# Optimization experiments

Hardware: AMD Instinct MI355X
Metric: run time of the kernel (lower is better)

The kernel has to match this reference:

```python
import jax, jax.numpy as jnp
import numpy as np


def log_g(x):
    # log of g(x) where g(x) = x + 0.5 for x >= 0 else sigmoid(x)
    return jnp.where(x >= 0, jnp.log(jnp.where(x >= 0, x, 0.0) + 0.5), -jax.nn.softplus(-x))


def mingru_layer(x, h0, W, b):
    # x: (B,S,Din), h0: (B,1,H) positive, W: (2H,Din), b: (2H,)
    gh = jnp.einsum('bsd,ed->bse', x, W) + b
    gate, hidden = jnp.split(gh, 2, axis=-1)
    log_z = -jax.nn.softplus(-gate)        # log sigmoid(gate)
    log_coeffs = -jax.nn.softplus(gate)    # log (1 - sigmoid(gate))
    log_values = jnp.concatenate([jnp.log(h0), log_z + log_g(hidden)], axis=1)  # (B,S+1,H)
    a_star = jnp.pad(jnp.cumsum(log_coeffs, axis=1), ((0, 0), (1, 0), (0, 0)))  # (B,S+1,H)
    log_h = a_star + jax.lax.cumlogsumexp(log_values - a_star, axis=1)
    return jnp.exp(log_h)[:, 1:]  # (B,S,H)


def setup_inputs() -> dict:
    key = jax.random.key(0)
    ks = jax.random.split(key, 6)
    B, S, D, H = 8, 2048, 1024, 1024
    L = 2
    s = 0.02
    return {
        'x': jax.random.normal(ks[0], (B, S, D), jnp.float32),
        'h': jax.random.uniform(ks[1], (L, B, 1, H), jnp.float32, 0.05, 1.0),
        'w0': jax.random.normal(ks[2], (2 * H, D), jnp.float32) * s,
        'b0': jax.random.normal(ks[3], (2 * H,), jnp.float32) * s,
        'w1': jax.random.normal(ks[4], (2 * H, H), jnp.float32) * s,
        'b1': jax.random.normal(ks[5], (2 * H,), jnp.float32) * s,
    }


def reference(x, h, w0, b0, w1, b1):
    # layer 0 (residual, align = Identity since input_dims == hidden_dims)
    out0 = mingru_layer(x, h[0], w0, b0)
    h0_final = out0[:, -1:]
    inp = out0 + x
    # layer 1 (last layer: residual, no dropout after)
    out1 = mingru_layer(inp, h[1], w1, b1)
    h1_final = out1[:, -1:]
    out = out1 + inp
    h_final = jnp.stack([h0_final, h1_final])  # (L,B,1,H)
    return out, h_final
```

## Files before the change

kernel.cpp:

```cpp
#include <hip/hip_runtime.h>
#include <hip/hip_bf16.h>
#include <cstdint>
#include <cstddef>

#define GAS __attribute__((address_space(1)))
#define LAS __attribute__((address_space(3)))

typedef __attribute__((ext_vector_type(8))) __bf16 bf16x8;
typedef __attribute__((ext_vector_type(4))) float f32x4;

constexpr int kB = 8, kS = 2048, kK = 1024, kH = 1024;
constexpr int kM = kB * kS;
constexpr int kN2 = 2 * kH;
constexpr int kChunks = 64;
constexpr int kSc = kS / kChunks;

constexpr size_t kOffXb   = 0;
constexpr size_t kOffW0   = 33554432;
constexpr size_t kOffW1   = 37748736;
constexpr size_t kOffA    = 41943040;
constexpr size_t kOffG    = 75497472;
constexpr size_t kOffCA   = 109051904;
constexpr size_t kOffCV   = 111149056;
constexpr size_t kOffHst  = 113246208;
constexpr size_t kWsNeed  = 115343360;

__device__ __forceinline__ ushort f2bf(float f) {
    union { float f; uint32_t u; } v; v.f = f;
    uint32_t r = v.u + 0x7FFFu + ((v.u >> 16) & 1u);
    return (ushort)(r >> 16);
}
__device__ __forceinline__ float bf2f(ushort u) {
    union { uint32_t u; float f; } v; v.u = (uint32_t)u << 16;
    return v.f;
}

__global__ void cvt_bf16_kernel(const float* __restrict__ src, ushort* __restrict__ dst, int n4) {
    int i = blockIdx.x * blockDim.x + threadIdx.x;
    if (i >= n4) return;
    f32x4 v = *reinterpret_cast<const f32x4*>(src + (size_t)i * 4);
    ushort4 o;
    o.x = f2bf(v.x); o.y = f2bf(v.y); o.z = f2bf(v.z); o.w = f2bf(v.w);
    *reinterpret_cast<ushort4*>(dst + (size_t)i * 4) = o;
}

__global__ __launch_bounds__(256, 2)
void gemm_epi_kernel(const ushort* __restrict__ A, const ushort* __restrict__ W,
                     const float* __restrict__ bias,
                     ushort* __restrict__ abuf, ushort* __restrict__ gbuf)
{
    __shared__ ushort As[128 * 64];
    __shared__ ushort Bs[128 * 64];

    const int tid  = threadIdx.x;
    const int lane = tid & 63;
    const int wv   = tid >> 6;
    const int bid  = blockIdx.x;
    const int tn   = bid & 15;
    const int tm   = bid >> 4;
    const int m0   = tm * 128;
    const int n0   = tn * 128;
    const int wm   = wv & 1, wn = wv >> 1;

    f32x4 acc[4][4];
#pragma unroll
    for (int i = 0; i < 4; ++i)
#pragma unroll
        for (int j = 0; j < 4; ++j) acc[i][j] = (f32x4){0.f, 0.f, 0.f, 0.f};

    const int srow = tid >> 3;
    const int scol = (tid & 7) * 8;
    const size_t a_base = (size_t)(m0 + srow) * kK + scol;
    const size_t b_base = (size_t)(n0 + srow) * kK + scol;

    for (int kt = 0; kt < kK / 64; ++kt) {
        const int k0 = kt * 64;
#pragma unroll
        for (int i = 0; i < 4; ++i) {
            const ushort* gp = A + a_base + (size_t)i * 32 * kK + k0;
            __builtin_amdgcn_global_load_lds((const GAS void*)gp,
                (LAS void*)((char*)As + i * 4096 + wv * 1024), 16, 0, 0);
        }
#pragma unroll
        for (int i = 0; i < 4; ++i) {
            const ushort* gp = W + b_base + (size_t)i * 32 * kK + k0;
            __builtin_amdgcn_global_load_lds((const GAS void*)gp,
                (LAS void*)((char*)Bs + i * 4096 + wv * 1024), 16, 0, 0);
        }
        __syncthreads();
#pragma unroll
        for (int ks = 0; ks < 2; ++ks) {
            bf16x8 af[4], bfr[4];
#pragma unroll
            for (int mr = 0; mr < 4; ++mr) {
                int off = (wm * 64 + mr * 16 + (lane & 15)) * 64 + ks * 32 + (lane >> 4) * 8;
                af[mr] = *reinterpret_cast<const bf16x8*>(&As[off]);
            }
#pragma unroll
            for (int nr = 0; nr < 4; ++nr) {
                int off = (wn * 64 + nr * 16 + (lane & 15)) * 64 + ks * 32 + (lane >> 4) * 8;
                bfr[nr] = *reinterpret_cast<const bf16x8*>(&Bs[off]);
            }
#pragma unroll
            for (int mr = 0; mr < 4; ++mr)
#pragma unroll
                for (int nr = 0; nr < 4; ++nr)
                    acc[mr][nr] = __builtin_amdgcn_mfma_f32_16x16x32_bf16(af[mr], bfr[nr], acc[mr][nr], 0, 0, 0);
        }
        __syncthreads();
    }

    const bool isGate = (tn < 8);
    ushort* outp = isGate ? abuf : gbuf;
    const int nb_local = (isGate ? tn : tn - 8) * 128 + wn * 64;
    float bn[4];
#pragma unroll
    for (int nr = 0; nr < 4; ++nr) bn[nr] = bias[n0 + wn * 64 + nr * 16 + (lane & 15)];
#pragma unroll
    for (int mr = 0; mr < 4; ++mr) {
#pragma unroll
        for (int i = 0; i < 4; ++i) {
            const int m = m0 + wm * 64 + mr * 16 + (lane >> 4) * 4 + i;
            ushort* rowp = outp + (size_t)m * kH + nb_local;
#pragma unroll
            for (int nr = 0; nr < 4; ++nr) {
                float val = acc[mr][nr][i] + bn[nr];
                float r;
                if (isGate) r = 1.f / (1.f + __expf(val));
                else        r = (val >= 0.f) ? val + 0.5f : 1.f / (1.f + __expf(-val));
                rowp[nr * 16 + (lane & 15)] = f2bf(r);
            }
        }
    }
}

__global__ void scan_reduce_kernel(const ushort* __restrict__ abuf, const ushort* __restrict__ gbuf,
                                   float* __restrict__ cA, float* __restrict__ cV)
{
    int idx = blockIdx.x * 256 + threadIdx.x;
    int chg = idx & 255;
    int c   = (idx >> 8) & (kChunks - 1);
    int b   = idx >> 14;
    size_t ch = (size_t)chg * 4;
    size_t row = (size_t)b * kS + (size_t)c * kSc;
    const ushort* ap = abuf + row * kH + ch;
    const ushort* gp = gbuf + row * kH + ch;
    f32x4 A = (f32x4){1.f, 1.f, 1.f, 1.f};
    f32x4 V = (f32x4){0.f, 0.f, 0.f, 0.f};
    for (int t = 0; t < kSc; ++t) {
        ushort4 au = *reinterpret_cast<const ushort4*>(ap);
        ushort4 gu = *reinterpret_cast<const ushort4*>(gp);
        f32x4 a = (f32x4){bf2f(au.x), bf2f(au.y), bf2f(au.z), bf2f(au.w)};
        f32x4 g = (f32x4){bf2f(gu.x), bf2f(gu.y), bf2f(gu.z), bf2f(gu.w)};
        V = a * V + (1.f - a) * g;
        A = A * a;
        ap += kH; gp += kH;
    }
    size_t o = ((size_t)(b * kChunks + c) * kH) + ch;
    *reinterpret_cast<f32x4*>(cA + o) = A;
    *reinterpret_cast<f32x4*>(cV + o) = V;
}

__global__ void scan_chunks_kernel(const float* __restrict__ cA, const float* __restrict__ cV,
                                   const float* __restrict__ h0, float* __restrict__ hstart,
                                   float* __restrict__ hfin)
{
    int idx = blockIdx.x * 256 + threadIdx.x;
    int chg = idx & 255;
    int b   = idx >> 8;
    size_t ch = (size_t)chg * 4;
    f32x4 h = *reinterpret_cast<const f32x4*>(h0 + (size_t)b * kH + ch);
    for (int c = 0; c < kChunks; ++c) {
        size_t o = ((size_t)(b * kChunks + c) * kH) + ch;
        *reinterpret_cast<f32x4*>(hstart + o) = h;
        f32x4 A = *reinterpret_cast<const f32x4*>(cA + o);
        f32x4 V = *reinterpret_cast<const f32x4*>(cV + o);
        h = A * h + V;
    }
    *reinterpret_cast<f32x4*>(hfin + (size_t)b * kH + ch) = h;
}

template<bool L1>
__global__ void scan_apply_kernel(const ushort* __restrict__ abuf, const ushort* __restrict__ gbuf,
                                  const float* __restrict__ hstart, const void* __restrict__ addin,
                                  void* __restrict__ outp)
{
    int idx = blockIdx.x * 256 + threadIdx.x;
    int chg = idx & 255;
    int c   = (idx >> 8) & (kChunks - 1);
    int b   = idx >> 14;
    size_t ch = (size_t)chg * 4;
    size_t row = (size_t)b * kS + (size_t)c * kSc;
    size_t base = row * kH + ch;
    f32x4 h = *reinterpret_cast<const f32x4*>(hstart + ((size_t)(b * kChunks + c) * kH) + ch);
    const ushort* ap = abuf + base;
    const ushort* gp = gbuf + base;
    for (int t = 0; t < kSc; ++t) {
        ushort4 au = *reinterpret_cast<const ushort4*>(ap);
        ushort4 gu = *reinterpret_cast<const ushort4*>(gp);
        f32x4 a = (f32x4){bf2f(au.x), bf2f(au.y), bf2f(au.z), bf2f(au.w)};
        f32x4 g = (f32x4){bf2f(gu.x), bf2f(gu.y), bf2f(gu.z), bf2f(gu.w)};
        h = a * h + (1.f - a) * g;
        f32x4 r;
        if (L1) {
            ushort4 xu = *reinterpret_cast<const ushort4*>((const ushort*)addin + base + (size_t)t * kH);
            r = (f32x4){bf2f(xu.x), bf2f(xu.y), bf2f(xu.z), bf2f(xu.w)};
        } else {
            r = *reinterpret_cast<const f32x4*>((const float*)addin + base + (size_t)t * kH);
        }
        f32x4 o = h + r;
        if (L1) {
            *reinterpret_cast<f32x4*>((float*)outp + base + (size_t)t * kH) = o;
        } else {
            ushort4 ob;
            ob.x = f2bf(o.x); ob.y = f2bf(o.y); ob.z = f2bf(o.z); ob.w = f2bf(o.w);
            *reinterpret_cast<ushort4*>((ushort*)outp + base + (size_t)t * kH) = ob;
        }
        ap += kH; gp += kH;
    }
}

extern "C" void kernel_launch(void* const* d_in, const int* in_sizes, int n_in,
                              void* d_out, int out_size, void* d_ws, size_t ws_size,
                              hipStream_t stream)
{
    const float* x  = (const float*)d_in[0];
    const float* h  = (const float*)d_in[1];
    const float* w0 = (const float*)d_in[2];
    const float* b0 = (const float*)d_in[3];
    const float* w1 = (const float*)d_in[4];
    const float* b1 = (const float*)d_in[5];
    float* out = (float*)d_out;
    char* ws = (char*)d_ws;

    if (ws_size < kWsNeed) return;

    ushort* xb   = (ushort*)(ws + kOffXb);
    ushort* inpb = (ushort*)(ws + kOffXb);
    ushort* w0b  = (ushort*)(ws + kOffW0);
    ushort* w1b  = (ushort*)(ws + kOffW1);
    ushort* abuf = (ushort*)(ws + kOffA);
    ushort* gbuf = (ushort*)(ws + kOffG);
    float*  cA   = (float*)(ws + kOffCA);
    float*  cV   = (float*)(ws + kOffCV);
    float*  hst  = (float*)(ws + kOffHst);

    float* out_h = out + (size_t)kM * kH;

    cvt_bf16_kernel<<<(kM * kK / 4 + 255) / 256, 256, 0, stream>>>(x, xb, kM * kK / 4);
    cvt_bf16_kernel<<<(kN2 * kK / 4 + 255) / 256, 256, 0, stream>>>(w0, w0b, kN2 * kK / 4);
    cvt_bf16_kernel<<<(kN2 * kK / 4 + 255) / 256, 256, 0, stream>>>(w1, w1b, kN2 * kK / 4);

    gemm_epi_kernel<<<(kM / 128) * (kN2 / 128), 256, 0, stream>>>(xb, w0b, b0, abuf, gbuf);
    scan_reduce_kernel<<<512, 256, 0, stream>>>(abuf, gbuf, cA, cV);
    scan_chunks_kernel<<<8, 256, 0, stream>>>(cA, cV, h, hst, out_h);
    scan_apply_kernel<false><<<512, 256, 0, stream>>>(abuf, gbuf, hst, x, inpb);

    gemm_epi_kernel<<<(kM / 128) * (kN2 / 128), 256, 0, stream>>>(inpb, w1b, b1, abuf, gbuf);
    scan_reduce_kernel<<<512, 256, 0, stream>>>(abuf, gbuf, cA, cV);
    scan_chunks_kernel<<<8, 256, 0, stream>>>(cA, cV, h + (size_t)kB * kH, hst, out_h + (size_t)kB * kH);
    scan_apply_kernel<true><<<512, 256, 0, stream>>>(abuf, gbuf, hst, inpb, out);
}
```

Baseline: 300.6 us.

## Rewrite GEMM with 256x256 tiles, 4-stage LDS pipeline and grid swizzle

The bf16 GEMM goes from 128x128 tiles with a single-buffered LDS loop to 256x256 tiles on 512 threads. A 4-buffer ring of BK=32 stages is prefetched two steps ahead using manual vmcnt waits and one barrier per step, and the block-to-tile mapping is swizzled. The aim is to overlap global loads with MFMA work, raise arithmetic intensity per block, and improve L2 reuse. The cost is 128KB of LDS and many more accumulator registers, which may limit occupancy and increase epilogue register pressure.

```diff
diff --git a/kernel.cpp b/kernel.cpp
--- a/kernel.cpp
+++ b/kernel.cpp
@@ -14,6 +14,9 @@
 constexpr int kN2 = 2 * kH;
 constexpr int kChunks = 64;
 constexpr int kSc = kS / kChunks;
+
+constexpr int BM = 256, BN = 256, BK = 32;
+constexpr int NKT = kK / BK;
 
 constexpr size_t kOffXb   = 0;
 constexpr size_t kOffW0   = 33554432;
@@ -44,91 +47,113 @@
     *reinterpret_cast<ushort4*>(dst + (size_t)i * 4) = o;
 }
 
-__global__ __launch_bounds__(256, 2)
+__global__ __launch_bounds__(512, 2)
 void gemm_epi_kernel(const ushort* __restrict__ A, const ushort* __restrict__ W,
                      const float* __restrict__ bias,
                      ushort* __restrict__ abuf, ushort* __restrict__ gbuf)
 {
-    __shared__ ushort As[128 * 64];
-    __shared__ ushort Bs[128 * 64];
+    __shared__ ushort smem[65536];
 
     const int tid  = threadIdx.x;
     const int lane = tid & 63;
     const int wv   = tid >> 6;
-    const int bid  = blockIdx.x;
-    const int tn   = bid & 15;
-    const int tm   = bid >> 4;
-    const int m0   = tm * 128;
-    const int n0   = tn * 128;
-    const int wm   = wv & 1, wn = wv >> 1;
-
-    f32x4 acc[4][4];
-#pragma unroll
-    for (int i = 0; i < 4; ++i)
+    const int wm   = wv >> 2;
+    const int wn   = wv & 3;
+
+    const int bid = blockIdx.x;
+    const int sid = (bid & 7) * 64 + (bid >> 3);
+    const int tm  = sid >> 3;
+    const int tn  = sid & 7;
+    const int m0  = tm * BM;
+    const int n0  = tn * BN;
+
+    f32x4 acc[8][4];
+#pragma unroll
+    for (int i = 0; i < 8; ++i)
 #pragma unroll
         for (int j = 0; j < 4; ++j) acc[i][j] = (f32x4){0.f, 0.f, 0.f, 0.f};
 
-    const int srow = tid >> 3;
-    const int scol = (tid & 7) * 8;
-    const size_t a_base = (size_t)(m0 + srow) * kK + scol;
-    const size_t b_base = (size_t)(n0 + srow) * kK + scol;
-
-    for (int kt = 0; kt < kK / 64; ++kt) {
-        const int k0 = kt * 64;
+    const int srow = wv * 16 + (lane >> 2);
+    const int scol = (lane & 3) * 8;
+
+#define STAGE(t_) do {                                                          \
+    const int buf_ = (t_) & 3;                                                  \
+    const int k0_  = (t_) * BK;                                                 \
+    ushort* la_ = smem + buf_ * 16384;                                          \
+    ushort* lb_ = la_ + 8192;                                                   \
+    _Pragma("unroll")                                                           \
+    for (int i_ = 0; i_ < 2; ++i_) {                                            \
+        const ushort* ga_ = A + (size_t)(m0 + i_ * 128 + srow) * kK + k0_ + scol; \
+        __builtin_amdgcn_global_load_lds((const GAS void*)ga_,                  \
+            (LAS void*)((char*)(la_ + i_ * 4096 + wv * 512)), 16, 0, 0);        \
+        const ushort* gb_ = W + (size_t)(n0 + i_ * 128 + srow) * kK + k0_ + scol; \
+        __builtin_amdgcn_global_load_lds((const GAS void*)gb_,                  \
+            (LAS void*)((char*)(lb_ + i_ * 4096 + wv * 512)), 16, 0, 0);        \
+    } } while (0)
+
+#define COMPUTE(t_) do {                                                        \
+    const int buf_ = (t_) & 3;                                                  \
+    const ushort* la_ = smem + buf_ * 16384 + wm * 128 * 32                     \
+                        + (lane & 15) * 32 + (lane >> 4) * 8;                   \
+    const ushort* lb_ = smem + buf_ * 16384 + 8192 + wn * 64 * 32               \
+                        + (lane & 15) * 32 + (lane >> 4) * 8;                   \
+    bf16x8 af_[8], bf_[4];                                                      \
+    _Pragma("unroll")                                                           \
+    for (int mf_ = 0; mf_ < 8; ++mf_)                                           \
+        af_[mf_] = *reinterpret_cast<const bf16x8*>(la_ + mf_ * 512);           \
+    _Pragma("unroll")                                                           \
+    for (int nf_ = 0; nf_ < 4; ++nf_)                                           \
+        bf_[nf_] = *reinterpret_cast<const bf16x8*>(lb_ + nf_ * 512);           \
+    __builtin_amdgcn_s_setprio(1);                                              \
+    _Pragma("unroll")                                                           \
+    for (int mf_ = 0; mf_ < 8; ++mf_)                                           \
+        _Pragma("unroll")                                                       \
+        for (int nf_ = 0; nf_ < 4; ++nf_)                                       \
+            acc[mf_][nf_] = __builtin_amdgcn_mfma_f32_16x16x32_bf16(            \
+                af_[mf_], bf_[nf_], acc[mf_][nf_], 0, 0, 0);                    \
+    __builtin_amdgcn_s_setprio(0);                                              \
+    } while (0)
+
+    STAGE(0);
+    STAGE(1);
+    for (int t = 0; t < NKT - 2; ++t) {
+        asm volatile("s_waitcnt vmcnt(4)" ::: "memory");
+        __builtin_amdgcn_s_barrier();
+        __builtin_amdgcn_sched_barrier(0);
+        STAGE(t + 2);
+        COMPUTE(t);
+    }
+    asm volatile("s_waitcnt vmcnt(4)" ::: "memory");
+    __builtin_amdgcn_s_barrier();
+    __builtin_amdgcn_sched_barrier(0);
+    COMPUTE(NKT - 2);
+    asm volatile("s_waitcnt vmcnt(0)" ::: "memory");
+    __builtin_amdgcn_s_barrier();
+    __builtin_amdgcn_sched_barrier(0);
+    COMPUTE(NKT - 1);
+
+#undef STAGE
+#undef COMPUTE
+
+    const bool isGate = (tn < 4);
+    ushort* outp = isGate ? abuf : gbuf;
+    const int ncol0 = (isGate ? tn : tn - 4) * 256 + wn * 64;
+    float bn[4];
+#pragma unroll
+    for (int nf = 0; nf < 4; ++nf) bn[nf] = bias[n0 + wn * 64 + nf * 16 + (lane & 15)];
+#pragma unroll
+    for (int mf = 0; mf < 8; ++mf) {
 #pragma unroll
         for (int i = 0; i < 4; ++i) {
-            const ushort* gp = A + a_base + (size_t)i * 32 * kK + k0;
-            __builtin_amdgcn_global_load_lds((const GAS void*)gp,
-                (LAS void*)((char*)As + i * 4096 + wv * 1024), 16, 0, 0);
-        }
-#pragma unroll
-        for (int i = 0; i < 4; ++i) {
-            const ushort* gp = W + b_base + (size_t)i * 32 * kK + k0;
-            __builtin_amdgcn_global_load_lds((const GAS void*)gp,
-                (LAS void*)((char*)Bs + i * 4096 + wv * 1024), 16, 0, 0);
-        }
-        __syncthreads();
-#pragma unroll
-        for (int ks = 0; ks < 2; ++ks) {
-            bf16x8 af[4], bfr[4];
-#pragma unroll
-            for (int mr = 0; mr < 4; ++mr) {
-                int off = (wm * 64 + mr * 16 + (lane & 15)) * 64 + ks * 32 + (lane >> 4) * 8;
-                af[mr] = *reinterpret_cast<const bf16x8*>(&As[off]);
-            }
-#pragma unroll
-            for (int nr = 0; nr < 4; ++nr) {
-                int off = (wn * 64 + nr * 16 + (lane & 15)) * 64 + ks * 32 + (lane >> 4) * 8;
-                bfr[nr] = *reinterpret_cast<const bf16x8*>(&Bs[off]);
-            }
-#pragma unroll
-            for (int mr = 0; mr < 4; ++mr)
-#pragma unroll
-                for (int nr = 0; nr < 4; ++nr)
-                    acc[mr][nr] = __builtin_amdgcn_mfma_f32_16x16x32_bf16(af[mr], bfr[nr], acc[mr][nr], 0, 0, 0);
-        }
-        __syncthreads();
-    }
-
-    const bool isGate = (tn < 8);
-    ushort* outp = isGate ? abuf : gbuf;
-    const int nb_local = (isGate ? tn : tn - 8) * 128 + wn * 64;
-    float bn[4];
-#pragma unroll
-    for (int nr = 0; nr < 4; ++nr) bn[nr] = bias[n0 + wn * 64 + nr * 16 + (lane & 15)];
-#pragma unroll
-    for (int mr = 0; mr < 4; ++mr) {
-#pragma unroll
-        for (int i = 0; i < 4; ++i) {
-            const int m = m0 + wm * 64 + mr * 16 + (lane >> 4) * 4 + i;
-            ushort* rowp = outp + (size_t)m * kH + nb_local;
-#pragma unroll
-            for (int nr = 0; nr < 4; ++nr) {
-                float val = acc[mr][nr][i] + bn[nr];
+            const int m = m0 + wm * 128 + mf * 16 + (lane >> 4) * 4 + i;
+            ushort* rowp = outp + (size_t)m * kH + ncol0;
+#pragma unroll
+            for (int nf = 0; nf < 4; ++nf) {
+                float val = acc[mf][nf][i] + bn[nf];
                 float r;
                 if (isGate) r = 1.f / (1.f + __expf(val));
                 else        r = (val >= 0.f) ? val + 0.5f : 1.f / (1.f + __expf(-val));
-                rowp[nr * 16 + (lane & 15)] = f2bf(r);
+                rowp[nf * 16 + (lane & 15)] = f2bf(r);
             }
         }
     }
@@ -251,12 +276,14 @@
     cvt_bf16_kernel<<<(kN2 * kK / 4 + 255) / 256, 256, 0, stream>>>(w0, w0b, kN2 * kK / 4);
     cvt_bf16_kernel<<<(kN2 * kK / 4 + 255) / 256, 256, 0, stream>>>(w1, w1b, kN2 * kK / 4);
 
-    gemm_epi_kernel<<<(kM / 128) * (kN2 / 128), 256, 0, stream>>>(xb, w0b, b0, abuf, gbuf);
+    const int gemm_grid = (kM / BM) * (kN2 / BN);
+
+    gemm_epi_kernel<<<gemm_grid, 512, 0, stream>>>(xb, w0b, b0, abuf, gbuf);
     scan_reduce_kernel<<<512, 256, 0, stream>>>(abuf, gbuf, cA, cV);
     scan_chunks_kernel<<<8, 256, 0, stream>>>(cA, cV, h, hst, out_h);
     scan_apply_kernel<false><<<512, 256, 0, stream>>>(abuf, gbuf, hst, x, inpb);
 
-    gemm_epi_kernel<<<(kM / 128) * (kN2 / 128), 256, 0, stream>>>(inpb, w1b, b1, abuf, gbuf);
+    gemm_epi_kernel<<<gemm_grid, 512, 0, stream>>>(inpb, w1b, b1, abuf, gbuf);
     scan_reduce_kernel<<<512, 256, 0, stream>>>(abuf, gbuf, cA, cV);
     scan_chunks_kernel<<<8, 256, 0, stream>>>(cA, cV, h + (size_t)kB * kH, hst, out_h + (size_t)kB * kH);
     scan_apply_kernel<true><<<512, 256, 0, stream>>>(abuf, gbuf, hst, inpb, out);
```

After: 299.6 us. Within noise of the previous version (-0.3%).
